# Optimization experiments

Hardware: AMD Instinct MI355X
Metric: run time of the kernel (lower is better)

## Reference

```python
import math
import jax, jax.numpy as jnp
import numpy as np

B, S, H = 4, 2048, 1024

def setup_inputs() -> dict:
    key = jax.random.key(0)
    k1, k2, k3, k4 = jax.random.split(key, 4)
    X = jax.random.normal(k1, (B, S, H), dtype=jnp.float32)
    attention_mask = jax.random.randint(k2, (B, S), 0, 2).astype(jnp.bool_)
    W = jax.random.normal(k3, (H, 3 * H), dtype=jnp.float32) * (1.0 / math.sqrt(H))
    b = jax.random.normal(k4, (3 * H,), dtype=jnp.float32) * 0.02
    return {"X": X, "attention_mask": attention_mask, "W": W, "b": b}

def reference(X, attention_mask, W, b):
    hidden_dim = X.shape[-1]
    # fused QKV projection: (B,S,3H)
    QKV = X @ W + b
    Q, K, V = jnp.split(QKV, 3, axis=-1)
    # scores: (B, S, S)
    scores = jnp.einsum('bqd,bkd->bqk', Q, K) / math.sqrt(hidden_dim)
    # 2D key-padding mask (B,S) -> broadcast over query dim; True = masked
    mask = attention_mask[:, None, :]  # (B,1,S) broadcasts to (B,S,S)
    scores = jnp.where(mask, -jnp.inf, scores)
    attn = jax.nn.softmax(scores, axis=-1)
    # dropout_rate = 0.0 (eval): identity
    return jnp.einsum('bqk,bkd->bqd', attn, V)
```

## Files before the change

kernel.cpp:

```cpp
#include <hip/hip_runtime.h>
#include <hip/hip_bf16.h>
#include <stdint.h>


typedef __attribute__((ext_vector_type(8))) short bf16x8;
typedef __attribute__((ext_vector_type(4))) float f32x4;

__device__ __forceinline__ void async_cp16(const void* g, void* l) {
  __builtin_amdgcn_global_load_lds(
      (const __attribute__((address_space(1))) void*)g,
      (__attribute__((address_space(3))) void*)l, 16, 0, 0);
}

__device__ __forceinline__ uint32_t laddr(const void* p) {
  return (uint32_t)(uintptr_t)(const __attribute__((address_space(3))) void*)p;
}

#define FENCE() asm volatile("" ::: "memory")
#define BAR()                           \
  do {                                  \
    FENCE();                            \
    __builtin_amdgcn_s_barrier();       \
    FENCE();                            \
  } while (0)
#define VMW(N) asm volatile("s_waitcnt vmcnt(" #N ")" ::: "memory")
#define LGKM0()                                            \
  do {                                                     \
    asm volatile("s_waitcnt lgkmcnt(0)" ::: "memory");     \
    __builtin_amdgcn_sched_barrier(0);                     \
  } while (0)
#define DSR(dst, a, OFF) \
  asm volatile("ds_read_b128 %0, %1 offset:" #OFF : "=v"(dst) : "v"(a))

__global__ void cvt_f32_bf16(const float* __restrict__ s,
                             __hip_bfloat16* __restrict__ d, int n) {
  int i = (blockIdx.x * blockDim.x + threadIdx.x) * 4;
  if (i >= n) return;
  float4 f = *(const float4*)(s + i);
  __hip_bfloat16 o[4];
  o[0] = __float2bfloat16(f.x);
  o[1] = __float2bfloat16(f.y);
  o[2] = __float2bfloat16(f.z);
  o[3] = __float2bfloat16(f.w);
  *(ushort4*)(d + i) = *(const ushort4*)o;
}

__global__ void transpose_cvt_f32(const float* __restrict__ src, int srcld,
                                  __hip_bfloat16* __restrict__ dst, int dstld) {
  __shared__ float tile[32][33];
  int bx = blockIdx.x * 32;
  int by = blockIdx.y * 32;
  int tx = threadIdx.x, ty = threadIdx.y;
#pragma unroll
  for (int j = 0; j < 4; ++j)
    tile[ty + j * 8][tx] = src[(int64_t)(by + ty + j * 8) * srcld + bx + tx];
  __syncthreads();
#pragma unroll
  for (int j = 0; j < 4; ++j)
    dst[(int64_t)(bx + ty + j * 8) * dstld + by + tx] =
        __float2bfloat16(tile[tx][ty + j * 8]);
}

__global__ __launch_bounds__(256) void mask_scan(const int* __restrict__ mask,
                                                 int* __restrict__ idx,
                                                 int* __restrict__ cnt,
                                                 int* __restrict__ cnt_pad) {
  const int b = blockIdx.x;
  mask += b * 2048;
  idx += b * 2048;
  const int t = threadIdx.x;
  const int lane = t & 63, wave = t >> 6;

  int keep[8];
  int local = 0;
#pragma unroll
  for (int j = 0; j < 8; ++j) {
    keep[j] = (mask[t * 8 + j] == 0);
    local += keep[j];
  }
  int pre = local;
#pragma unroll
  for (int off = 1; off <= 32; off <<= 1) {
    int n = __shfl_up(pre, off, 64);
    if (lane >= off) pre += n;
  }
  __shared__ int wsum[4];
  if (lane == 63) wsum[wave] = pre;
  __syncthreads();
  int base = 0;
  for (int w = 0; w < wave; ++w) base += wsum[w];
  int excl = base + pre - local;
#pragma unroll
  for (int j = 0; j < 8; ++j)
    if (keep[j]) idx[excl++] = t * 8 + j;
  if (t == 255) {
    int tot = base + pre;
    cnt[b] = tot;
    cnt_pad[b] = (tot + 127) & ~127;
  }
}

__global__ __launch_bounds__(256) void gemm_qkv(
    const __hip_bfloat16* __restrict__ Xb, const __hip_bfloat16* __restrict__ Wt,
    const float* __restrict__ bias, const int* __restrict__ idx,
    const int* __restrict__ cnt, const int* __restrict__ cnt_pad,
    __hip_bfloat16* __restrict__ Q, __hip_bfloat16* __restrict__ Kc,
    __hip_bfloat16* __restrict__ Vt) {
  const int z = blockIdx.z;
  const int f = blockIdx.x;
  const int xcd = f & 7, loc = f >> 3;
  const int m0 = ((loc & 7) * 2 + (xcd >> 2)) * 128;
  const int n_idx = (loc >> 3) * 4 + (xcd & 3);
  const bool isQ = (n_idx < 8);
  if (!isQ && m0 >= cnt_pad[z]) return;
  const int n0 = (isQ ? n_idx : n_idx - 8) * 128;
  const __hip_bfloat16* A = Xb + (int64_t)z * 2048 * 1024;
  const __hip_bfloat16* Bt = Wt + (isQ ? 0 : (int64_t)1024 * 1024);
  const float* bv = bias + (isQ ? 0 : 1024);

  const int tid = threadIdx.x;
  const int wave = tid >> 6, lane = tid & 63;
  const int quad = lane >> 4, tr = lane & 15, t7 = tr & 7;
  const int wm = wave & 1, wn = wave >> 1;

  __shared__ __hip_bfloat16 ls[32768];

  const __hip_bfloat16* gsrc[8];
  int loff[8];
  {
    const int srow = lane >> 3;
    const int kcs = (((lane & 7) ^ srow) * 8);
    const int cz = isQ ? 0 : cnt[z];
    const int* idxz = idx + z * 2048;
#pragma unroll
    for (int cc = 0; cc < 8; ++cc) {
      int c = wave * 8 + cc;
      int isA = (c < 16);
      int cr = isA ? c : (c - 16);
      int row = cr * 8 + srow;
      if (isA) {
        int ar = m0 + row;
        if (!isQ) ar = (ar < cz) ? idxz[ar] : 0;
        gsrc[cc] = A + (int64_t)ar * 1024 + kcs;
      } else {
        gsrc[cc] = Bt + (int64_t)(n0 + row) * 1024 + kcs;
      }
      loff[cc] = (isA ? 0 : 8192) + cr * 512;
    }
  }

  uint32_t aAd[2][2], bBd[2][2];
  {
    uint32_t base = laddr(ls);
#pragma unroll
    for (int b = 0; b < 2; ++b)
#pragma unroll
      for (int w = 0; w < 2; ++w) {
        uint32_t col = (uint32_t)(((((w << 2) | quad)) ^ t7) * 16);
        aAd[b][w] = base + b * 32768 + (wm * 64 + tr) * 128 + col;
        bBd[b][w] = base + b * 32768 + 16384 + (wn * 64 + tr) * 128 + col;
      }
  }

  f32x4 acc[4][4];
#pragma unroll
  for (int mi = 0; mi < 4; ++mi)
#pragma unroll
    for (int ni = 0; ni < 4; ++ni) acc[mi][ni] = (f32x4){0.f, 0.f, 0.f, 0.f};

  bf16x8 af[4], bf[4];

#define STAGE(BUF, k0)                                            \
  do {                                                            \
    _Pragma("unroll") for (int cc = 0; cc < 8; ++cc)              \
        async_cp16(gsrc[cc] + (k0), ls + (BUF)*16384 + loff[cc]); \
  } while (0)
#define COMP(BUF)                                                             \
  do {                                                                        \
    _Pragma("unroll") for (int w = 0; w < 2; ++w) {                           \
      DSR(af[0], aAd[BUF][w], 0);                                             \
      DSR(af[1], aAd[BUF][w], 2048);                                          \
      DSR(af[2], aAd[BUF][w], 4096);                                          \
      DSR(af[3], aAd[BUF][w], 6144);                                          \
      DSR(bf[0], bBd[BUF][w], 0);                                             \
      DSR(bf[1], bBd[BUF][w], 2048);                                          \
      DSR(bf[2], bBd[BUF][w], 4096);                                          \
      DSR(bf[3], bBd[BUF][w], 6144);                                          \
      LGKM0();                                                                \
      _Pragma("unroll") for (int mi = 0; mi < 4; ++mi)                        \
          _Pragma("unroll") for (int ni = 0; ni < 4; ++ni) acc[mi][ni] =      \
              __builtin_amdgcn_mfma_f32_16x16x32_bf16(af[mi], bf[ni],         \
                                                      acc[mi][ni], 0, 0, 0);  \
    }                                                                         \
  } while (0)

  STAGE(0, 0);
  for (int it = 0; it < 8; ++it) {
    STAGE(1, (2 * it + 1) * 64);
    VMW(8); BAR();
    COMP(0);
    BAR();
    if (it < 7) {
      STAGE(0, (2 * it + 2) * 64);
      VMW(8);
    } else {
      VMW(0);
    }
    BAR();
    COMP(1);
    BAR();
  }
#undef STAGE
#undef COMP

  const int rowbase = m0 + wm * 64;
  const int colbase = n0 + wn * 64;
  if (isQ) {
    __hip_bfloat16* C = Q + (int64_t)z * 2048 * 1024;
#pragma unroll
    for (int ni = 0; ni < 4; ++ni) {
      int col = colbase + ni * 16 + tr;
      float bb = bv[col];
#pragma unroll
      for (int mi = 0; mi < 4; ++mi) {
        int row = rowbase + mi * 16 + quad * 4;
#pragma unroll
        for (int r = 0; r < 4; ++r)
          C[(int64_t)(row + r) * 1024 + col] =
              __float2bfloat16(acc[mi][ni][r] + bb);
      }
    }
  } else if (n0 < 1024) {
    __hip_bfloat16* C = Kc + (int64_t)z * 2048 * 1024;
#pragma unroll
    for (int ni = 0; ni < 4; ++ni) {
      int col = colbase + ni * 16 + tr;
      float bb = bv[col];
#pragma unroll
      for (int mi = 0; mi < 4; ++mi) {
        int row = rowbase + mi * 16 + quad * 4;
#pragma unroll
        for (int r = 0; r < 4; ++r)
          C[(int64_t)(row + r) * 1024 + col] =
              __float2bfloat16(acc[mi][ni][r] + bb);
      }
    }
  } else {
    __syncthreads();
#pragma unroll
    for (int ni = 0; ni < 4; ++ni) {
      int cl = wn * 64 + ni * 16 + tr;
      float bb = bv[colbase + ni * 16 + tr];
#pragma unroll
      for (int mi = 0; mi < 4; ++mi) {
        int rl = wm * 64 + mi * 16 + quad * 4;
        __hip_bfloat16 h[4];
#pragma unroll
        for (int r = 0; r < 4; ++r) h[r] = __float2bfloat16(acc[mi][ni][r] + bb);
        *(ushort4*)(ls + cl * 136 + rl) = *(const ushort4*)h;
      }
    }
    __syncthreads();
    __hip_bfloat16* Vz = Vt + (int64_t)z * 1024 * 2048;
    const int d0 = n0 - 1024;
    const int seg = tid & 15;
#pragma unroll
    for (int p = 0; p < 8; ++p) {
      int d = p * 16 + (tid >> 4);
      bf16x8 v = *(const bf16x8*)(ls + d * 136 + seg * 8);
      *(bf16x8*)(Vz + (int64_t)(d0 + d) * 2048 + m0 + seg * 8) = v;
    }
  }
}

__global__ __launch_bounds__(256) void gemm_scores(
    const __hip_bfloat16* __restrict__ Qb, const __hip_bfloat16* __restrict__ Kc,
    __hip_bfloat16* __restrict__ Sc, float* __restrict__ rowsum,
    const int* __restrict__ cnt, const int* __restrict__ cnt_pad,
    float scale2) {
  const int z = blockIdx.z;
  const int f = blockIdx.x;
  const int xcd = f & 7, loc = f >> 3;
  const int m0 = ((loc & 7) * 2 + (xcd >> 2)) * 128;
  const int n0 = ((loc >> 3) * 4 + (xcd & 3)) * 128;
  if (n0 >= cnt_pad[z]) return;
  const __hip_bfloat16* A = Qb + (int64_t)z * 2048 * 1024;
  const __hip_bfloat16* Bt = Kc + (int64_t)z * 2048 * 1024;

  const int tid = threadIdx.x;
  const int wave = tid >> 6, lane = tid & 63;
  const int quad = lane >> 4, tr = lane & 15, t7 = tr & 7;
  const int wm = wave & 1, wn = wave >> 1;

  __shared__ __hip_bfloat16 ls[32768];

  const __hip_bfloat16* gsrc[8];
  int loff[8];
  {
    const int srow = lane >> 3;
    const int kcs = (((lane & 7) ^ srow) * 8);
#pragma unroll
    for (int cc = 0; cc < 8; ++cc) {
      int c = wave * 8 + cc;
      int isA = (c < 16);
      int cr = isA ? c : (c - 16);
      int row = cr * 8 + srow;
      gsrc[cc] = isA ? (A + (int64_t)(m0 + row) * 1024 + kcs)
                     : (Bt + (int64_t)(n0 + row) * 1024 + kcs);
      loff[cc] = (isA ? 0 : 8192) + cr * 512;
    }
  }

  uint32_t aAd[2][2], bBd[2][2];
  {
    uint32_t base = laddr(ls);
#pragma unroll
    for (int b = 0; b < 2; ++b)
#pragma unroll
      for (int w = 0; w < 2; ++w) {
        uint32_t col = (uint32_t)(((((w << 2) | quad)) ^ t7) * 16);
        aAd[b][w] = base + b * 32768 + (wm * 64 + tr) * 128 + col;
        bBd[b][w] = base + b * 32768 + 16384 + (wn * 64 + tr) * 128 + col;
      }
  }

  f32x4 acc[4][4];
#pragma unroll
  for (int mi = 0; mi < 4; ++mi)
#pragma unroll
    for (int ni = 0; ni < 4; ++ni) acc[mi][ni] = (f32x4){0.f, 0.f, 0.f, 0.f};

  bf16x8 af[4], bf[4];

#define STAGE(BUF, k0)                                            \
  do {                                                            \
    _Pragma("unroll") for (int cc = 0; cc < 8; ++cc)              \
        async_cp16(gsrc[cc] + (k0), ls + (BUF)*16384 + loff[cc]); \
  } while (0)
#define COMP(BUF)                                                             \
  do {                                                                        \
    _Pragma("unroll") for (int w = 0; w < 2; ++w) {                           \
      DSR(af[0], aAd[BUF][w], 0);                                             \
      DSR(af[1], aAd[BUF][w], 2048);                                          \
      DSR(af[2], aAd[BUF][w], 4096);                                          \
      DSR(af[3], aAd[BUF][w], 6144);                                          \
      DSR(bf[0], bBd[BUF][w], 0);                                             \
      DSR(bf[1], bBd[BUF][w], 2048);                                          \
      DSR(bf[2], bBd[BUF][w], 4096);                                          \
      DSR(bf[3], bBd[BUF][w], 6144);                                          \
      LGKM0();                                                                \
      _Pragma("unroll") for (int mi = 0; mi < 4; ++mi)                        \
          _Pragma("unroll") for (int ni = 0; ni < 4; ++ni) acc[mi][ni] =      \
              __builtin_amdgcn_mfma_f32_16x16x32_bf16(af[mi], bf[ni],         \
                                                      acc[mi][ni], 0, 0, 0);  \
    }                                                                         \
  } while (0)

  STAGE(0, 0);
  for (int it = 0; it < 8; ++it) {
    STAGE(1, (2 * it + 1) * 64);
    VMW(8); BAR();
    COMP(0);
    BAR();
    if (it < 7) {
      STAGE(0, (2 * it + 2) * 64);
      VMW(8);
    } else {
      VMW(0);
    }
    BAR();
    COMP(1);
    BAR();
  }
#undef STAGE
#undef COMP

  const int rowbase = m0 + wm * 64;
  const int colbase = n0 + wn * 64;
  const int cn = cnt[z];
  __hip_bfloat16* C = Sc + (int64_t)z * 2048 * 2048;

  float psum[4][4];
#pragma unroll
  for (int mi = 0; mi < 4; ++mi)
#pragma unroll
    for (int r = 0; r < 4; ++r) psum[mi][r] = 0.f;

#pragma unroll
  for (int ni = 0; ni < 4; ++ni) {
    int col = colbase + ni * 16 + tr;
    bool valid = (col < cn);
#pragma unroll
    for (int mi = 0; mi < 4; ++mi) {
      int row = rowbase + mi * 16 + quad * 4;
#pragma unroll
      for (int r = 0; r < 4; ++r) {
        float e = valid ? exp2f(acc[mi][ni][r] * scale2) : 0.f;
        C[(int64_t)(row + r) * 2048 + col] = __float2bfloat16(e);
        psum[mi][r] += e;
      }
    }
  }
#pragma unroll
  for (int off = 1; off <= 8; off <<= 1)
#pragma unroll
    for (int mi = 0; mi < 4; ++mi)
#pragma unroll
      for (int r = 0; r < 4; ++r)
        psum[mi][r] += __shfl_xor(psum[mi][r], off, 64);
  if (tr == 0) {
    float* rs = rowsum + z * 2048 + rowbase;
#pragma unroll
    for (int mi = 0; mi < 4; ++mi)
#pragma unroll
      for (int r = 0; r < 4; ++r)
        atomicAdd(&rs[mi * 16 + quad * 4 + r], psum[mi][r]);
  }
}

__global__ __launch_bounds__(256) void gemm_pv(
    const __hip_bfloat16* __restrict__ Sc, const __hip_bfloat16* __restrict__ Vt,
    float* __restrict__ out, const float* __restrict__ rowsum,
    const int* __restrict__ cnt_pad) {
  const int z = blockIdx.z;
  const int f = blockIdx.x;
  const int xcd = f & 7, loc = f >> 3;
  const int m0 = ((loc & 7) * 2 + (xcd >> 2)) * 128;
  const int n0 = ((loc >> 3) * 4 + (xcd & 3)) * 128;
  const int Ks = cnt_pad[z];
  const __hip_bfloat16* A = Sc + (int64_t)z * 2048 * 2048;
  const __hip_bfloat16* Bt = Vt + (int64_t)z * 1024 * 2048;

  const int tid = threadIdx.x;
  const int wave = tid >> 6, lane = tid & 63;
  const int quad = lane >> 4, tr = lane & 15, t7 = tr & 7;
  const int wm = wave & 1, wn = wave >> 1;

  __shared__ __hip_bfloat16 ls[32768];

  const __hip_bfloat16* gsrc[8];
  int loff[8];
  {
    const int srow = lane >> 3;
    const int kcs = (((lane & 7) ^ srow) * 8);
#pragma unroll
    for (int cc = 0; cc < 8; ++cc) {
      int c = wave * 8 + cc;
      int isA = (c < 16);
      int cr = isA ? c : (c - 16);
      int row = cr * 8 + srow;
      gsrc[cc] = isA ? (A + (int64_t)(m0 + row) * 2048 + kcs)
                     : (Bt + (int64_t)(n0 + row) * 2048 + kcs);
      loff[cc] = (isA ? 0 : 8192) + cr * 512;
    }
  }

  uint32_t aAd[2][2], bBd[2][2];
  {
    uint32_t base = laddr(ls);
#pragma unroll
    for (int b = 0; b < 2; ++b)
#pragma unroll
      for (int w = 0; w < 2; ++w) {
        uint32_t col = (uint32_t)(((((w << 2) | quad)) ^ t7) * 16);
        aAd[b][w] = base + b * 32768 + (wm * 64 + tr) * 128 + col;
        bBd[b][w] = base + b * 32768 + 16384 + (wn * 64 + tr) * 128 + col;
      }
  }

  f32x4 acc[4][4];
#pragma unroll
  for (int mi = 0; mi < 4; ++mi)
#pragma unroll
    for (int ni = 0; ni < 4; ++ni) acc[mi][ni] = (f32x4){0.f, 0.f, 0.f, 0.f};

  bf16x8 af[4], bf[4];

#define STAGE(BUF, k0)                                            \
  do {                                                            \
    _Pragma("unroll") for (int cc = 0; cc < 8; ++cc)              \
        async_cp16(gsrc[cc] + (k0), ls + (BUF)*16384 + loff[cc]); \
  } while (0)
#define COMP(BUF)                                                             \
  do {                                                                        \
    _Pragma("unroll") for (int w = 0; w < 2; ++w) {                           \
      DSR(af[0], aAd[BUF][w], 0);                                             \
      DSR(af[1], aAd[BUF][w], 2048);                                          \
      DSR(af[2], aAd[BUF][w], 4096);                                          \
      DSR(af[3], aAd[BUF][w], 6144);                                          \
      DSR(bf[0], bBd[BUF][w], 0);                                             \
      DSR(bf[1], bBd[BUF][w], 2048);                                          \
      DSR(bf[2], bBd[BUF][w], 4096);                                          \
      DSR(bf[3], bBd[BUF][w], 6144);                                          \
      LGKM0();                                                                \
      _Pragma("unroll") for (int mi = 0; mi < 4; ++mi)                        \
          _Pragma("unroll") for (int ni = 0; ni < 4; ++ni) acc[mi][ni] =      \
              __builtin_amdgcn_mfma_f32_16x16x32_bf16(af[mi], bf[ni],         \
                                                      acc[mi][ni], 0, 0, 0);  \
    }                                                                         \
  } while (0)

  const int NP = Ks >> 7;
  STAGE(0, 0);
  for (int it = 0; it < NP; ++it) {
    STAGE(1, (2 * it + 1) * 64);
    VMW(8); BAR();
    COMP(0);
    BAR();
    if (it + 1 < NP) {
      STAGE(0, (2 * it + 2) * 64);
      VMW(8);
    } else {
      VMW(0);
    }
    BAR();
    COMP(1);
    BAR();
  }
#undef STAGE
#undef COMP

  const int rowbase = m0 + wm * 64;
  const int colbase = n0 + wn * 64;
  const float* rs = rowsum + z * 2048 + rowbase;
  float invv[4][4];
#pragma unroll
  for (int mi = 0; mi < 4; ++mi)
#pragma unroll
    for (int r = 0; r < 4; ++r) invv[mi][r] = 1.0f / rs[mi * 16 + quad * 4 + r];

  float* C = out + (int64_t)z * 2048 * 1024;
#pragma unroll
  for (int ni = 0; ni < 4; ++ni) {
    int col = colbase + ni * 16 + tr;
#pragma unroll
    for (int mi = 0; mi < 4; ++mi) {
      int row = rowbase + mi * 16 + quad * 4;
#pragma unroll
      for (int r = 0; r < 4; ++r)
        C[(int64_t)(row + r) * 1024 + col] = acc[mi][ni][r] * invv[mi][r];
    }
  }
}

extern "C" void kernel_launch(void* const* d_in, const int* in_sizes, int n_in,
                              void* d_out, int out_size, void* d_ws,
                              size_t ws_size, hipStream_t stream) {
  const float* X = (const float*)d_in[0];
  const int* mask = (const int*)d_in[1];
  const float* W = (const float*)d_in[2];
  const float* bias = (const float*)d_in[3];
  float* out = (float*)d_out;

  char* ws = (char*)d_ws;
  auto alloc = [&](size_t bytes) {
    char* p = ws;
    ws += (bytes + 255) & ~(size_t)255;
    return p;
  };
  __hip_bfloat16* Xb = (__hip_bfloat16*)alloc(8192ULL * 1024 * 2);
  __hip_bfloat16* Wt = (__hip_bfloat16*)alloc(3072ULL * 1024 * 2);
  __hip_bfloat16* Q = (__hip_bfloat16*)alloc(8192ULL * 1024 * 2);
  __hip_bfloat16* Kc = (__hip_bfloat16*)alloc(4ULL * 2048 * 1024 * 2);
  __hip_bfloat16* Vt = (__hip_bfloat16*)alloc(4ULL * 1024 * 2048 * 2);
  __hip_bfloat16* Sc = (__hip_bfloat16*)alloc(4ULL * 2048 * 2048 * 2);
  float* rowsum = (float*)alloc(8192ULL * 4);
  int* idx = (int*)alloc(4ULL * 2048 * 4);
  int* cnt = (int*)alloc(64);
  int* cnt_pad = (int*)alloc(64);

  hipMemsetAsync(rowsum, 0, 8192ULL * 4, stream);
  cvt_f32_bf16<<<8192, 256, 0, stream>>>(X, Xb, 8192 * 1024);
  transpose_cvt_f32<<<dim3(96, 32, 1), dim3(32, 8), 0, stream>>>(W, 3072, Wt,
                                                                 1024);
  mask_scan<<<4, 256, 0, stream>>>(mask, idx, cnt, cnt_pad);
  gemm_qkv<<<dim3(384, 1, 4), 256, 0, stream>>>(Xb, Wt, bias, idx, cnt,
                                                cnt_pad, Q, Kc, Vt);
  gemm_scores<<<dim3(256, 1, 4), 256, 0, stream>>>(
      Q, Kc, Sc, rowsum, cnt, cnt_pad, 0.03125f * 1.4426950408889634f);
  gemm_pv<<<dim3(128, 1, 4), 256, 0, stream>>>(Sc, Vt, out, rowsum, cnt_pad);
}
```

Before: 204.7 us.

## Drop LDS double buffering in GEMMs to raise occupancy to four blocks per CU

Replaces the double-buffered async LDS staging in the QKV, scores and PV GEMM kernels with a single buffer, using a barrier, load, full wait and compute sequence each K step. This halves shared memory per block, and launch bounds now request four blocks per CU, so latency is meant to be hidden by more resident blocks instead of in-block prefetch. The cost is that each block now fully serializes global loads with MFMA compute, and the extra barriers add overhead. The launch-bounds hint may also limit registers available for the 64-float accumulator.

```diff
diff --git a/kernel.cpp b/kernel.cpp
--- a/kernel.cpp
+++ b/kernel.cpp
@@ -24,10 +24,10 @@
     FENCE();                            \
   } while (0)
 #define VMW(N) asm volatile("s_waitcnt vmcnt(" #N ")" ::: "memory")
-#define LGKM0()                                            \
-  do {                                                     \
-    asm volatile("s_waitcnt lgkmcnt(0)" ::: "memory");     \
-    __builtin_amdgcn_sched_barrier(0);                     \
+#define LGKM0()                                               \
+  do {                                                        \
+    asm volatile("s_waitcnt lgkmcnt(0)" ::: "memory");        \
+    __builtin_amdgcn_sched_barrier(0);                        \
   } while (0)
 #define DSR(dst, a, OFF) \
   asm volatile("ds_read_b128 %0, %1 offset:" #OFF : "=v"(dst) : "v"(a))
@@ -100,7 +100,7 @@
   }
 }
 
-__global__ __launch_bounds__(256) void gemm_qkv(
+__global__ __launch_bounds__(256, 4) void gemm_qkv(
     const __hip_bfloat16* __restrict__ Xb, const __hip_bfloat16* __restrict__ Wt,
     const float* __restrict__ bias, const int* __restrict__ idx,
     const int* __restrict__ cnt, const int* __restrict__ cnt_pad,
@@ -123,7 +123,7 @@
   const int quad = lane >> 4, tr = lane & 15, t7 = tr & 7;
   const int wm = wave & 1, wn = wave >> 1;
 
-  __shared__ __hip_bfloat16 ls[32768];
+  __shared__ __hip_bfloat16 ls[17408];
 
   const __hip_bfloat16* gsrc[8];
   int loff[8];
@@ -149,17 +149,15 @@
     }
   }
 
-  uint32_t aAd[2][2], bBd[2][2];
+  uint32_t aAd[2], bBd[2];
   {
     uint32_t base = laddr(ls);
 #pragma unroll
-    for (int b = 0; b < 2; ++b)
-#pragma unroll
-      for (int w = 0; w < 2; ++w) {
-        uint32_t col = (uint32_t)(((((w << 2) | quad)) ^ t7) * 16);
-        aAd[b][w] = base + b * 32768 + (wm * 64 + tr) * 128 + col;
-        bBd[b][w] = base + b * 32768 + 16384 + (wn * 64 + tr) * 128 + col;
-      }
+    for (int w = 0; w < 2; ++w) {
+      uint32_t col = (uint32_t)(((((w << 2) | quad)) ^ t7) * 16);
+      aAd[w] = base + (wm * 64 + tr) * 128 + col;
+      bBd[w] = base + 16384 + (wn * 64 + tr) * 128 + col;
+    }
   }
 
   f32x4 acc[4][4];
@@ -170,22 +168,22 @@
 
   bf16x8 af[4], bf[4];
 
-#define STAGE(BUF, k0)                                            \
-  do {                                                            \
-    _Pragma("unroll") for (int cc = 0; cc < 8; ++cc)              \
-        async_cp16(gsrc[cc] + (k0), ls + (BUF)*16384 + loff[cc]); \
-  } while (0)
-#define COMP(BUF)                                                             \
+#define STAGE(k0)                                     \
+  do {                                                \
+    _Pragma("unroll") for (int cc = 0; cc < 8; ++cc)  \
+        async_cp16(gsrc[cc] + (k0), ls + loff[cc]);   \
+  } while (0)
+#define COMP()                                                                \
   do {                                                                        \
     _Pragma("unroll") for (int w = 0; w < 2; ++w) {                           \
-      DSR(af[0], aAd[BUF][w], 0);                                             \
-      DSR(af[1], aAd[BUF][w], 2048);                                          \
-      DSR(af[2], aAd[BUF][w], 4096);                                          \
-      DSR(af[3], aAd[BUF][w], 6144);                                          \
-      DSR(bf[0], bBd[BUF][w], 0);                                             \
-      DSR(bf[1], bBd[BUF][w], 2048);                                          \
-      DSR(bf[2], bBd[BUF][w], 4096);                                          \
-      DSR(bf[3], bBd[BUF][w], 6144);                                          \
+      DSR(af[0], aAd[w], 0);                                                  \
+      DSR(af[1], aAd[w], 2048);                                               \
+      DSR(af[2], aAd[w], 4096);                                               \
+      DSR(af[3], aAd[w], 6144);                                               \
+      DSR(bf[0], bBd[w], 0);                                                  \
+      DSR(bf[1], bBd[w], 2048);                                               \
+      DSR(bf[2], bBd[w], 4096);                                               \
+      DSR(bf[3], bBd[w], 6144);                                               \
       LGKM0();                                                                \
       _Pragma("unroll") for (int mi = 0; mi < 4; ++mi)                        \
           _Pragma("unroll") for (int ni = 0; ni < 4; ++ni) acc[mi][ni] =      \
@@ -194,21 +192,12 @@
     }                                                                         \
   } while (0)
 
-  STAGE(0, 0);
-  for (int it = 0; it < 8; ++it) {
-    STAGE(1, (2 * it + 1) * 64);
-    VMW(8); BAR();
-    COMP(0);
+  for (int t = 0; t < 16; ++t) {
     BAR();
-    if (it < 7) {
-      STAGE(0, (2 * it + 2) * 64);
-      VMW(8);
-    } else {
-      VMW(0);
-    }
+    STAGE(t * 64);
+    VMW(0);
     BAR();
-    COMP(1);
-    BAR();
+    COMP();
   }
 #undef STAGE
 #undef COMP
@@ -273,7 +262,7 @@
   }
 }
 
-__global__ __launch_bounds__(256) void gemm_scores(
+__global__ __launch_bounds__(256, 4) void gemm_scores(
     const __hip_bfloat16* __restrict__ Qb, const __hip_bfloat16* __restrict__ Kc,
     __hip_bfloat16* __restrict__ Sc, float* __restrict__ rowsum,
     const int* __restrict__ cnt, const int* __restrict__ cnt_pad,
@@ -292,7 +281,7 @@
   const int quad = lane >> 4, tr = lane & 15, t7 = tr & 7;
   const int wm = wave & 1, wn = wave >> 1;
 
-  __shared__ __hip_bfloat16 ls[32768];
+  __shared__ __hip_bfloat16 ls[16384];
 
   const __hip_bfloat16* gsrc[8];
   int loff[8];
@@ -311,17 +300,15 @@
     }
   }
 
-  uint32_t aAd[2][2], bBd[2][2];
+  uint32_t aAd[2], bBd[2];
   {
     uint32_t base = laddr(ls);
 #pragma unroll
-    for (int b = 0; b < 2; ++b)
-#pragma unroll
-      for (int w = 0; w < 2; ++w) {
-        uint32_t col = (uint32_t)(((((w << 2) | quad)) ^ t7) * 16);
-        aAd[b][w] = base + b * 32768 + (wm * 64 + tr) * 128 + col;
-        bBd[b][w] = base + b * 32768 + 16384 + (wn * 64 + tr) * 128 + col;
-      }
+    for (int w = 0; w < 2; ++w) {
+      uint32_t col = (uint32_t)(((((w << 2) | quad)) ^ t7) * 16);
+      aAd[w] = base + (wm * 64 + tr) * 128 + col;
+      bBd[w] = base + 16384 + (wn * 64 + tr) * 128 + col;
+    }
   }
 
   f32x4 acc[4][4];
@@ -332,22 +319,22 @@
 
   bf16x8 af[4], bf[4];
 
-#define STAGE(BUF, k0)                                            \
-  do {                                                            \
-    _Pragma("unroll") for (int cc = 0; cc < 8; ++cc)              \
-        async_cp16(gsrc[cc] + (k0), ls + (BUF)*16384 + loff[cc]); \
-  } while (0)
-#define COMP(BUF)                                                             \
+#define STAGE(k0)                                     \
+  do {                                                \
+    _Pragma("unroll") for (int cc = 0; cc < 8; ++cc)  \
+        async_cp16(gsrc[cc] + (k0), ls + loff[cc]);   \
+  } while (0)
+#define COMP()                                                                \
   do {                                                                        \
     _Pragma("unroll") for (int w = 0; w < 2; ++w) {                           \
-      DSR(af[0], aAd[BUF][w], 0);                                             \
-      DSR(af[1], aAd[BUF][w], 2048);                                          \
-      DSR(af[2], aAd[BUF][w], 4096);                                          \
-      DSR(af[3], aAd[BUF][w], 6144);                                          \
-      DSR(bf[0], bBd[BUF][w], 0);                                             \
-      DSR(bf[1], bBd[BUF][w], 2048);                                          \
-      DSR(bf[2], bBd[BUF][w], 4096);                                          \
-      DSR(bf[3], bBd[BUF][w], 6144);                                          \
+      DSR(af[0], aAd[w], 0);                                                  \
+      DSR(af[1], aAd[w], 2048);                                               \
+      DSR(af[2], aAd[w], 4096);                                               \
+      DSR(af[3], aAd[w], 6144);                                               \
+      DSR(bf[0], bBd[w], 0);                                                  \
+      DSR(bf[1], bBd[w], 2048);                                               \
+      DSR(bf[2], bBd[w], 4096);                                               \
+      DSR(bf[3], bBd[w], 6144);                                               \
       LGKM0();                                                                \
       _Pragma("unroll") for (int mi = 0; mi < 4; ++mi)                        \
           _Pragma("unroll") for (int ni = 0; ni < 4; ++ni) acc[mi][ni] =      \
@@ -356,21 +343,12 @@
     }                                                                         \
   } while (0)
 
-  STAGE(0, 0);
-  for (int it = 0; it < 8; ++it) {
-    STAGE(1, (2 * it + 1) * 64);
-    VMW(8); BAR();
-    COMP(0);
+  for (int t = 0; t < 16; ++t) {
     BAR();
-    if (it < 7) {
-      STAGE(0, (2 * it + 2) * 64);
-      VMW(8);
-    } else {
-      VMW(0);
-    }
+    STAGE(t * 64);
+    VMW(0);
     BAR();
-    COMP(1);
-    BAR();
+    COMP();
   }
 #undef STAGE
 #undef COMP
@@ -418,7 +396,7 @@
   }
 }
 
-__global__ __launch_bounds__(256) void gemm_pv(
+__global__ __launch_bounds__(256, 4) void gemm_pv(
     const __hip_bfloat16* __restrict__ Sc, const __hip_bfloat16* __restrict__ Vt,
     float* __restrict__ out, const float* __restrict__ rowsum,
     const int* __restrict__ cnt_pad) {
@@ -436,7 +414,7 @@
   const int quad = lane >> 4, tr = lane & 15, t7 = tr & 7;
   const int wm = wave & 1, wn = wave >> 1;
 
-  __shared__ __hip_bfloat16 ls[32768];
+  __shared__ __hip_bfloat16 ls[16384];
 
   const __hip_bfloat16* gsrc[8];
   int loff[8];
@@ -455,17 +433,15 @@
     }
   }
 
-  uint32_t aAd[2][2], bBd[2][2];
+  uint32_t aAd[2], bBd[2];
   {
     uint32_t base = laddr(ls);
 #pragma unroll
-    for (int b = 0; b < 2; ++b)
-#pragma unroll
-      for (int w = 0; w < 2; ++w) {
-        uint32_t col = (uint32_t)(((((w << 2) | quad)) ^ t7) * 16);
-        aAd[b][w] = base + b * 32768 + (wm * 64 + tr) * 128 + col;
-        bBd[b][w] = base + b * 32768 + 16384 + (wn * 64 + tr) * 128 + col;
-      }
+    for (int w = 0; w < 2; ++w) {
+      uint32_t col = (uint32_t)(((((w << 2) | quad)) ^ t7) * 16);
+      aAd[w] = base + (wm * 64 + tr) * 128 + col;
+      bBd[w] = base + 16384 + (wn * 64 + tr) * 128 + col;
+    }
   }
 
   f32x4 acc[4][4];
@@ -476,22 +452,22 @@
 
   bf16x8 af[4], bf[4];
 
-#define STAGE(BUF, k0)                                            \
-  do {                                                            \
-    _Pragma("unroll") for (int cc = 0; cc < 8; ++cc)              \
-        async_cp16(gsrc[cc] + (k0), ls + (BUF)*16384 + loff[cc]); \
-  } while (0)
-#define COMP(BUF)                                                             \
+#define STAGE(k0)                                     \
+  do {                                                \
+    _Pragma("unroll") for (int cc = 0; cc < 8; ++cc)  \
+        async_cp16(gsrc[cc] + (k0), ls + loff[cc]);   \
+  } while (0)
+#define COMP()                                                                \
   do {                                                                        \
     _Pragma("unroll") for (int w = 0; w < 2; ++w) {                           \
-      DSR(af[0], aAd[BUF][w], 0);                                             \
-      DSR(af[1], aAd[BUF][w], 2048);                                          \
-      DSR(af[2], aAd[BUF][w], 4096);                                          \
-      DSR(af[3], aAd[BUF][w], 6144);                                          \
-      DSR(bf[0], bBd[BUF][w], 0);                                             \
-      DSR(bf[1], bBd[BUF][w], 2048);                                          \
-      DSR(bf[2], bBd[BUF][w], 4096);                                          \
-      DSR(bf[3], bBd[BUF][w], 6144);                                          \
+      DSR(af[0], aAd[w], 0);                                                  \
+      DSR(af[1], aAd[w], 2048);                                               \
+      DSR(af[2], aAd[w], 4096);                                               \
+      DSR(af[3], aAd[w], 6144);                                               \
+      DSR(bf[0], bBd[w], 0);                                                  \
+      DSR(bf[1], bBd[w], 2048);                                               \
+      DSR(bf[2], bBd[w], 4096);                                               \
+      DSR(bf[3], bBd[w], 6144);                                               \
       LGKM0();                                                                \
       _Pragma("unroll") for (int mi = 0; mi < 4; ++mi)                        \
           _Pragma("unroll") for (int ni = 0; ni < 4; ++ni) acc[mi][ni] =      \
@@ -500,22 +476,13 @@
     }                                                                         \
   } while (0)
 
-  const int NP = Ks >> 7;
-  STAGE(0, 0);
-  for (int it = 0; it < NP; ++it) {
-    STAGE(1, (2 * it + 1) * 64);
-    VMW(8); BAR();
-    COMP(0);
+  const int NT = Ks >> 6;
+  for (int t = 0; t < NT; ++t) {
     BAR();
-    if (it + 1 < NP) {
-      STAGE(0, (2 * it + 2) * 64);
-      VMW(8);
-    } else {
-      VMW(0);
-    }
+    STAGE(t * 64);
+    VMW(0);
     BAR();
-    COMP(1);
-    BAR();
+    COMP();
   }
 #undef STAGE
 #undef COMP
```

Result: no change. 208.5 us (+1.9%).
